# Performance work log

Measured on AMD Instinct MI355X. Metric: run time of the kernel, lower is better.

Reference implementation:

```python
import jax, jax.numpy as jnp
import numpy as np

WS = 8            # window_size
N = WS * WS       # tokens per window = 64
DIM = 512
H = 16            # num_heads
HD = DIM // H     # head_dim = 32
P = 16            # linformer proj_dim
B = 2048          # number of windows (batch * windows per image)


def _relative_position_index(ws: int) -> np.ndarray:
    coords = np.stack(np.meshgrid(np.arange(ws), np.arange(ws), indexing='ij'))  # [2,ws,ws]
    cf = coords.reshape(2, -1)                                                   # [2, N]
    rel = cf[:, :, None] - cf[:, None, :]                                        # [2, N, N]
    rel = rel.transpose(1, 2, 0).astype(np.int64)                                # [N, N, 2]
    rel[:, :, 0] += ws - 1
    rel[:, :, 1] += ws - 1
    rel[:, :, 0] *= 2 * ws - 1
    return rel.sum(-1)  # [N, N]

REL_INDEX = jnp.asarray(_relative_position_index(WS))  # int, [N, N]


def setup_inputs() -> dict:
    key = jax.random.key(0)
    ks = jax.random.split(key, 9)
    s = 0.02
    return {
        'x': jax.random.normal(ks[0], (B, N, DIM), dtype=jnp.float32),
        'w_qkv': jax.random.normal(ks[1], (DIM, 3 * DIM), dtype=jnp.float32) * s,
        'b_qkv': jax.random.normal(ks[2], (3 * DIM,), dtype=jnp.float32) * s,
        'w_proj': jax.random.normal(ks[3], (DIM, DIM), dtype=jnp.float32) * s,
        'b_proj': jax.random.normal(ks[4], (DIM,), dtype=jnp.float32) * s,
        'w_k': jax.random.normal(ks[5], (P, N), dtype=jnp.float32) * s,   # Linear(N -> P), torch weight layout [out,in]
        'w_v': jax.random.normal(ks[6], (P, N), dtype=jnp.float32) * s,
        'bias_table': jax.random.normal(ks[7], ((2 * WS - 1) ** 2, H), dtype=jnp.float32) * s,
    }


def reference(x, w_qkv, b_qkv, w_proj, b_proj, w_k, w_v, bias_table):
    B_, n, c = x.shape
    scale = HD ** -0.5
    qkv = (x @ w_qkv + b_qkv).reshape(B_, n, 3, H, HD)
    qkv = jnp.transpose(qkv, (2, 0, 3, 1, 4))          # [3, B, H, N, hd]
    q, k, v = qkv[0] * scale, qkv[1], qkv[2]           # each [B, H, N, hd]
    # Linformer projection along token axis N -> P
    k = jnp.einsum('bhnd,pn->bhpd', k, w_k)            # [B, H, P, hd]
    v = jnp.einsum('bhnd,pn->bhpd', v, w_v)            # [B, H, P, hd]
    attn = jnp.einsum('bhnd,bhpd->bhnp', q, k)         # [B, H, N, P]
    # relative position bias gather, sliced to projected length P
    bias = bias_table[REL_INDEX.reshape(-1)].reshape(n, n, H)  # [N, N, H]
    bias = jnp.transpose(bias, (2, 0, 1))[None, :, :, :attn.shape[-1]]  # [1, H, N, P]
    attn = jax.nn.softmax(attn + bias, axis=-1)
    out = jnp.einsum('bhnp,bhpd->bhnd', attn, v)       # [B, H, N, hd]
    out = jnp.transpose(out, (0, 2, 1, 3)).reshape(B_, n, c)
    return out @ w_proj + b_proj
```

## Files before the change

### kernel.cpp

```cpp
#include <hip/hip_runtime.h>

typedef __bf16 bf16;
typedef __attribute__((ext_vector_type(8))) __bf16 bf16x8;
typedef __attribute__((ext_vector_type(4))) __bf16 bf16x4;
typedef __attribute__((ext_vector_type(4))) float f32x4;
typedef __attribute__((ext_vector_type(4))) short s16x4;

#define SCALE 0.17677669529663687f

__device__ __forceinline__ f32x4 mfma16(bf16x8 a, bf16x8 b, f32x4 c) {
  return __builtin_amdgcn_mfma_f32_16x16x32_bf16(a, b, c, 0, 0, 0);
}

__device__ __forceinline__ f32x4 mfma16k16(bf16x4 a, bf16x4 b, f32x4 c) {
#if __has_builtin(__builtin_amdgcn_mfma_f32_16x16x16bf16_1k)
  return __builtin_amdgcn_mfma_f32_16x16x16bf16_1k(
      __builtin_bit_cast(s16x4, a), __builtin_bit_cast(s16x4, b), c, 0, 0, 0);
#else
  asm("v_mfma_f32_16x16x16_bf16 %0, %1, %2, %0" : "+v"(c) : "v"(a), "v"(b));
  return c;
#endif
}

__global__ void prep_weights(const float* __restrict__ w_qkv,
                             const float* __restrict__ w_proj,
                             bf16* __restrict__ wt, bf16* __restrict__ wpt) {
  __shared__ float tile[32][33];
  int b = blockIdx.x;
  const float* src; bf16* dst; int C, tk, tc;
  if (b < 768) {
    src = w_qkv; dst = wt; C = 1536; tk = (b & 15) * 32; tc = (b >> 4) * 32;
  } else {
    b -= 768; src = w_proj; dst = wpt; C = 512; tk = (b & 15) * 32; tc = (b >> 4) * 32;
  }
  int tx = threadIdx.x & 31, ty = threadIdx.x >> 5;
#pragma unroll
  for (int i = 0; i < 4; i++)
    tile[ty + i * 8][tx] = src[(size_t)(tk + ty + i * 8) * C + tc + tx];
  __syncthreads();
#pragma unroll
  for (int i = 0; i < 4; i++)
    dst[(size_t)(tc + ty + i * 8) * 512 + tk + tx] = (bf16)tile[tx][ty + i * 8];
}

__launch_bounds__(512, 2)
__global__ void ewattn(const float* __restrict__ x,
                       const float* __restrict__ b_qkv,
                       const float* __restrict__ w_k,
                       const float* __restrict__ w_v,
                       const float* __restrict__ bias_table,
                       const float* __restrict__ b_proj,
                       const bf16* __restrict__ wt,
                       const bf16* __restrict__ wpt,
                       float* __restrict__ out) {
  __shared__ bf16 xs[64][520];
  __shared__ bf16 xk[16][520];
  __shared__ bf16 xv[16][520];
  __shared__ bf16 wkl[16][72];
  __shared__ bf16 wvl[16][72];
  __shared__ float rs[32];
  __shared__ bf16 qs[8][64][40];
  __shared__ bf16 kps[8][16][40];

  const int tid  = threadIdx.x;
  const int lane = tid & 63;
  const int wid  = tid >> 6;
  const int l15  = lane & 15;
  const int quad = lane >> 4;
  const int win  = blockIdx.x;
  const float* xw = x + (size_t)win * (64 * 512);

  for (int i = tid; i < 64 * 64; i += 512) {
    int r = i >> 6, c8 = (i & 63) * 8;
    float4 v0 = *reinterpret_cast<const float4*>(xw + r * 512 + c8);
    float4 v1 = *reinterpret_cast<const float4*>(xw + r * 512 + c8 + 4);
    bf16x8 p;
    p[0] = (bf16)v0.x; p[1] = (bf16)v0.y; p[2] = (bf16)v0.z; p[3] = (bf16)v0.w;
    p[4] = (bf16)v1.x; p[5] = (bf16)v1.y; p[6] = (bf16)v1.z; p[7] = (bf16)v1.w;
    *reinterpret_cast<bf16x8*>(&xs[r][c8]) = p;
  }
  for (int i = tid; i < 1024; i += 512) {
    int p = i >> 6, n = i & 63;
    wkl[p][n] = (bf16)w_k[i];
    wvl[p][n] = (bf16)w_v[i];
  }
  if (tid < 16) {
    float sk = 0.f, sv = 0.f;
#pragma unroll
    for (int n = 0; n < 64; n++) { sk += w_k[tid * 64 + n]; sv += w_v[tid * 64 + n]; }
    rs[tid] = sk; rs[16 + tid] = sv;
  }
  __syncthreads();

  {
    f32x4 ak[4], av[4];
#pragma unroll
    for (int i = 0; i < 4; i++) { ak[i] = f32x4{0.f,0.f,0.f,0.f}; av[i] = f32x4{0.f,0.f,0.f,0.f}; }
#pragma unroll
    for (int kt = 0; kt < 2; kt++) {
      bf16x8 aK = *(const bf16x8*)&wkl[l15][kt * 32 + quad * 8];
      bf16x8 aV = *(const bf16x8*)&wvl[l15][kt * 32 + quad * 8];
      int n0 = kt * 32 + quad * 8;
#pragma unroll
      for (int nt = 0; nt < 4; nt++) {
        int c = wid * 64 + nt * 16 + l15;
        bf16x8 bb;
#pragma unroll
        for (int j = 0; j < 8; j++) bb[j] = xs[n0 + j][c];
        ak[nt] = mfma16(aK, bb, ak[nt]);
        av[nt] = mfma16(aV, bb, av[nt]);
      }
    }
#pragma unroll
    for (int nt = 0; nt < 4; nt++) {
      int c = wid * 64 + nt * 16 + l15;
#pragma unroll
      for (int r = 0; r < 4; r++) {
        xk[quad * 4 + r][c] = (bf16)ak[nt][r];
        xv[quad * 4 + r][c] = (bf16)av[nt][r];
      }
    }
  }

  bf16x4 qb[4][4];
  {
    f32x4 qacc[4][4];
#pragma unroll
    for (int nt = 0; nt < 4; nt++)
#pragma unroll
      for (int mt = 0; mt < 4; mt++) qacc[nt][mt] = f32x4{0.f,0.f,0.f,0.f};
    for (int kt = 0; kt < 16; kt++) {
      bf16x8 af[4];
#pragma unroll
      for (int mt = 0; mt < 4; mt++)
        af[mt] = *(const bf16x8*)&xs[mt * 16 + l15][kt * 32 + quad * 8];
#pragma unroll
      for (int nt = 0; nt < 4; nt++) {
        int c = wid * 64 + nt * 16 + l15;
        bf16x8 bb = *(const bf16x8*)&wt[(size_t)c * 512 + kt * 32 + quad * 8];
#pragma unroll
        for (int mt = 0; mt < 4; mt++)
          qacc[nt][mt] = mfma16(af[mt], bb, qacc[nt][mt]);
      }
    }
#pragma unroll
    for (int nt = 0; nt < 4; nt++) {
      float bq = b_qkv[wid * 64 + nt * 16 + l15];
#pragma unroll
      for (int mt = 0; mt < 4; mt++)
#pragma unroll
        for (int r = 0; r < 4; r++)
          qb[nt][mt][r] = (bf16)((qacc[nt][mt][r] + bq) * SCALE);
    }
  }
  __syncthreads();

  float rsk[4], rsv[4];
#pragma unroll
  for (int j = 0; j < 4; j++) { rsk[j] = rs[quad * 4 + j]; rsv[j] = rs[16 + quad * 4 + j]; }

  for (int hi = 0; hi < 2; hi++) {
    const int h = wid * 2 + hi;

    f32x4 kp[2], vp[2];
    kp[0] = kp[1] = vp[0] = vp[1] = f32x4{0.f,0.f,0.f,0.f};
    for (int kt = 0; kt < 16; kt++) {
      bf16x8 aK = *(const bf16x8*)&xk[l15][kt * 32 + quad * 8];
      bf16x8 aV = *(const bf16x8*)&xv[l15][kt * 32 + quad * 8];
#pragma unroll
      for (int nt = 0; nt < 2; nt++) {
        int ck = 512 + h * 32 + nt * 16 + l15;
        int cv = 1024 + h * 32 + nt * 16 + l15;
        bf16x8 bk = *(const bf16x8*)&wt[(size_t)ck * 512 + kt * 32 + quad * 8];
        bf16x8 bv = *(const bf16x8*)&wt[(size_t)cv * 512 + kt * 32 + quad * 8];
        kp[nt] = mfma16(aK, bk, kp[nt]);
        vp[nt] = mfma16(aV, bv, vp[nt]);
      }
    }
#pragma unroll
    for (int nt = 0; nt < 2; nt++) {
      float bk = b_qkv[512 + h * 32 + nt * 16 + l15];
#pragma unroll
      for (int r = 0; r < 4; r++)
        kps[wid][quad * 4 + r][nt * 16 + l15] = (bf16)(kp[nt][r] + rsk[r] * bk);
    }
    bf16x4 bvf[2];
#pragma unroll
    for (int nd = 0; nd < 2; nd++) {
      float bv = b_qkv[1024 + h * 32 + nd * 16 + l15];
#pragma unroll
      for (int j = 0; j < 4; j++)
        bvf[nd][j] = (bf16)(vp[nd][j] + rsv[j] * bv);
    }

#pragma unroll
    for (int nn = 0; nn < 2; nn++)
#pragma unroll
      for (int mt = 0; mt < 4; mt++)
#pragma unroll
        for (int r = 0; r < 4; r++)
          qs[wid][mt * 16 + quad * 4 + r][nn * 16 + l15] = qb[hi * 2 + nn][mt][r];

    f32x4 at[4];
    {
      bf16x8 bk2 = *(const bf16x8*)&kps[wid][l15][quad * 8];
#pragma unroll
      for (int mt = 0; mt < 4; mt++) {
        bf16x8 aq = *(const bf16x8*)&qs[wid][mt * 16 + l15][quad * 8];
        at[mt] = mfma16(aq, bk2, f32x4{0.f,0.f,0.f,0.f});
      }
    }

    float pr[4][4];
#pragma unroll
    for (int mt = 0; mt < 4; mt++) {
#pragma unroll
      for (int r = 0; r < 4; r++) {
        int n = mt * 16 + quad * 4 + r;
        int rel = ((n >> 3) - (l15 >> 3) + 7) * 15 + ((n & 7) - (l15 & 7) + 7);
        float e = __expf(at[mt][r] + bias_table[rel * 16 + h]);
        float s = e;
        s += __shfl_xor(s, 1); s += __shfl_xor(s, 2);
        s += __shfl_xor(s, 4); s += __shfl_xor(s, 8);
        pr[mt][r] = e * __builtin_amdgcn_rcpf(s);
      }
    }

#pragma unroll
    for (int mt = 0; mt < 4; mt++)
#pragma unroll
      for (int r = 0; r < 4; r++)
        qs[wid][mt * 16 + quad * 4 + r][l15] = (bf16)pr[mt][r];

    f32x4 ov[2][4];
#pragma unroll
    for (int mt = 0; mt < 4; mt++) {
      bf16x4 ap = *(const bf16x4*)&qs[wid][mt * 16 + l15][quad * 4];
#pragma unroll
      for (int nd = 0; nd < 2; nd++)
        ov[nd][mt] = mfma16k16(ap, bvf[nd], f32x4{0.f,0.f,0.f,0.f});
    }
#pragma unroll
    for (int nd = 0; nd < 2; nd++)
#pragma unroll
      for (int mt = 0; mt < 4; mt++)
#pragma unroll
        for (int r = 0; r < 4; r++)
          xs[mt * 16 + quad * 4 + r][h * 32 + nd * 16 + l15] = (bf16)ov[nd][mt][r];
  }
  __syncthreads();

  {
    f32x4 oacc[4][4];
#pragma unroll
    for (int nt = 0; nt < 4; nt++)
#pragma unroll
      for (int mt = 0; mt < 4; mt++) oacc[nt][mt] = f32x4{0.f,0.f,0.f,0.f};
    for (int kt = 0; kt < 16; kt++) {
      bf16x8 af[4];
#pragma unroll
      for (int mt = 0; mt < 4; mt++)
        af[mt] = *(const bf16x8*)&xs[mt * 16 + l15][kt * 32 + quad * 8];
#pragma unroll
      for (int nt = 0; nt < 4; nt++) {
        int c = wid * 64 + nt * 16 + l15;
        bf16x8 bb = *(const bf16x8*)&wpt[(size_t)c * 512 + kt * 32 + quad * 8];
#pragma unroll
        for (int mt = 0; mt < 4; mt++)
          oacc[nt][mt] = mfma16(af[mt], bb, oacc[nt][mt]);
      }
    }
    float* ow = out + (size_t)win * (64 * 512);
#pragma unroll
    for (int nt = 0; nt < 4; nt++) {
      int c = wid * 64 + nt * 16 + l15;
      float bp = b_proj[c];
#pragma unroll
      for (int mt = 0; mt < 4; mt++)
#pragma unroll
        for (int r = 0; r < 4; r++)
          ow[(size_t)(mt * 16 + quad * 4 + r) * 512 + c] = oacc[nt][mt][r] + bp;
    }
  }
}

extern "C" void kernel_launch(void* const* d_in, const int* in_sizes, int n_in,
                              void* d_out, int out_size, void* d_ws, size_t ws_size,
                              hipStream_t stream) {
  const float* x          = (const float*)d_in[0];
  const float* w_qkv      = (const float*)d_in[1];
  const float* b_qkv      = (const float*)d_in[2];
  const float* w_proj     = (const float*)d_in[3];
  const float* b_proj     = (const float*)d_in[4];
  const float* w_k        = (const float*)d_in[5];
  const float* w_v        = (const float*)d_in[6];
  const float* bias_table = (const float*)d_in[7];
  (void)in_sizes; (void)n_in; (void)out_size; (void)ws_size;

  bf16* wt  = (bf16*)d_ws;
  bf16* wpt = wt + 1536 * 512;

  prep_weights<<<1024, 256, 0, stream>>>(w_qkv, w_proj, wt, wpt);
  ewattn<<<2048, 512, 0, stream>>>(x, b_qkv, w_k, w_v, bias_table, b_proj,
                                   wt, wpt, (float*)d_out);
}
```

Baseline: 1.082 ms.

## Use 16 waves per window with one head per wave and register-resident attention

Doubles the block to 1024 threads so each wave owns one head and a 32-column slice of the QKV and output projections. It computes Q transposed (weights as the A operand), so the attention scores and the P·V product can be fed straight from MFMA accumulators in registers. This removes the per-wave qs/kps shared-memory staging and its round trips. The larger block halves per-wave register and tile work, but LDS use per block (~80KB for xs/xk/xv) may cap residency. The launch-bounds request of 4 blocks per CU may also force register spilling.

```diff
diff --git a/kernel.cpp b/kernel.cpp
--- a/kernel.cpp
+++ b/kernel.cpp
@@ -43,7 +43,7 @@
     dst[(size_t)(tc + ty + i * 8) * 512 + tk + tx] = (bf16)tile[tx][ty + i * 8];
 }
 
-__launch_bounds__(512, 2)
+__launch_bounds__(1024, 4)
 __global__ void ewattn(const float* __restrict__ x,
                        const float* __restrict__ b_qkv,
                        const float* __restrict__ w_k,
@@ -59,8 +59,6 @@
   __shared__ bf16 wkl[16][72];
   __shared__ bf16 wvl[16][72];
   __shared__ float rs[32];
-  __shared__ bf16 qs[8][64][40];
-  __shared__ bf16 kps[8][16][40];
 
   const int tid  = threadIdx.x;
   const int lane = tid & 63;
@@ -70,7 +68,7 @@
   const int win  = blockIdx.x;
   const float* xw = x + (size_t)win * (64 * 512);
 
-  for (int i = tid; i < 64 * 64; i += 512) {
+  for (int i = tid; i < 64 * 64; i += 1024) {
     int r = i >> 6, c8 = (i & 63) * 8;
     float4 v0 = *reinterpret_cast<const float4*>(xw + r * 512 + c8);
     float4 v1 = *reinterpret_cast<const float4*>(xw + r * 512 + c8 + 4);
@@ -79,10 +77,10 @@
     p[4] = (bf16)v1.x; p[5] = (bf16)v1.y; p[6] = (bf16)v1.z; p[7] = (bf16)v1.w;
     *reinterpret_cast<bf16x8*>(&xs[r][c8]) = p;
   }
-  for (int i = tid; i < 1024; i += 512) {
-    int p = i >> 6, n = i & 63;
-    wkl[p][n] = (bf16)w_k[i];
-    wvl[p][n] = (bf16)w_v[i];
+  {
+    int p = tid >> 6, n = tid & 63;
+    wkl[p][n] = (bf16)w_k[tid];
+    wvl[p][n] = (bf16)w_v[tid];
   }
   if (tid < 16) {
     float sk = 0.f, sv = 0.f;
@@ -93,17 +91,17 @@
   __syncthreads();
 
   {
-    f32x4 ak[4], av[4];
-#pragma unroll
-    for (int i = 0; i < 4; i++) { ak[i] = f32x4{0.f,0.f,0.f,0.f}; av[i] = f32x4{0.f,0.f,0.f,0.f}; }
+    f32x4 ak[2], av[2];
+#pragma unroll
+    for (int i = 0; i < 2; i++) { ak[i] = f32x4{0.f,0.f,0.f,0.f}; av[i] = f32x4{0.f,0.f,0.f,0.f}; }
 #pragma unroll
     for (int kt = 0; kt < 2; kt++) {
       bf16x8 aK = *(const bf16x8*)&wkl[l15][kt * 32 + quad * 8];
       bf16x8 aV = *(const bf16x8*)&wvl[l15][kt * 32 + quad * 8];
       int n0 = kt * 32 + quad * 8;
 #pragma unroll
-      for (int nt = 0; nt < 4; nt++) {
-        int c = wid * 64 + nt * 16 + l15;
+      for (int nt = 0; nt < 2; nt++) {
+        int c = wid * 32 + nt * 16 + l15;
         bf16x8 bb;
 #pragma unroll
         for (int j = 0; j < 8; j++) bb[j] = xs[n0 + j][c];
@@ -112,8 +110,8 @@
       }
     }
 #pragma unroll
-    for (int nt = 0; nt < 4; nt++) {
-      int c = wid * 64 + nt * 16 + l15;
+    for (int nt = 0; nt < 2; nt++) {
+      int c = wid * 32 + nt * 16 + l15;
 #pragma unroll
       for (int r = 0; r < 4; r++) {
         xk[quad * 4 + r][c] = (bf16)ak[nt][r];
@@ -122,164 +120,127 @@
     }
   }
 
-  bf16x4 qb[4][4];
-  {
-    f32x4 qacc[4][4];
-#pragma unroll
-    for (int nt = 0; nt < 4; nt++)
-#pragma unroll
-      for (int mt = 0; mt < 4; mt++) qacc[nt][mt] = f32x4{0.f,0.f,0.f,0.f};
+  bf16x4 qb[2][4];
+  {
+    f32x4 qacc[2][4];
+#pragma unroll
+    for (int ct = 0; ct < 2; ct++)
+#pragma unroll
+      for (int tt = 0; tt < 4; tt++) qacc[ct][tt] = f32x4{0.f,0.f,0.f,0.f};
+    for (int kt = 0; kt < 16; kt++) {
+      bf16x8 aw[2];
+#pragma unroll
+      for (int ct = 0; ct < 2; ct++)
+        aw[ct] = *(const bf16x8*)&wt[(size_t)(wid * 32 + ct * 16 + l15) * 512 + kt * 32 + quad * 8];
+      bf16x8 bx[4];
+#pragma unroll
+      for (int tt = 0; tt < 4; tt++)
+        bx[tt] = *(const bf16x8*)&xs[tt * 16 + l15][kt * 32 + quad * 8];
+#pragma unroll
+      for (int ct = 0; ct < 2; ct++)
+#pragma unroll
+        for (int tt = 0; tt < 4; tt++)
+          qacc[ct][tt] = mfma16(aw[ct], bx[tt], qacc[ct][tt]);
+    }
+#pragma unroll
+    for (int ct = 0; ct < 2; ct++)
+#pragma unroll
+      for (int tt = 0; tt < 4; tt++)
+#pragma unroll
+        for (int r = 0; r < 4; r++)
+          qb[ct][tt][r] = (bf16)((qacc[ct][tt][r] +
+                                  b_qkv[wid * 32 + ct * 16 + quad * 4 + r]) * SCALE);
+  }
+  __syncthreads();
+
+  const int h = wid;
+  f32x4 kpa[2], vpa[2];
+  kpa[0] = kpa[1] = vpa[0] = vpa[1] = f32x4{0.f,0.f,0.f,0.f};
+  for (int kt = 0; kt < 16; kt++) {
+    bf16x8 xkf = *(const bf16x8*)&xk[l15][kt * 32 + quad * 8];
+    bf16x8 xvf = *(const bf16x8*)&xv[l15][kt * 32 + quad * 8];
+#pragma unroll
+    for (int nt = 0; nt < 2; nt++) {
+      bf16x8 wkf = *(const bf16x8*)&wt[(size_t)(512  + h * 32 + nt * 16 + l15) * 512 + kt * 32 + quad * 8];
+      bf16x8 wvf = *(const bf16x8*)&wt[(size_t)(1024 + h * 32 + nt * 16 + l15) * 512 + kt * 32 + quad * 8];
+      kpa[nt] = mfma16(wkf, xkf, kpa[nt]);
+      vpa[nt] = mfma16(xvf, wvf, vpa[nt]);
+    }
+  }
+  float rskl = rs[l15];
+  float rsvr[4];
+#pragma unroll
+  for (int r = 0; r < 4; r++) rsvr[r] = rs[16 + quad * 4 + r];
+  bf16x4 kpf[2], bvf[2];
+#pragma unroll
+  for (int nt = 0; nt < 2; nt++) {
+    float bvb = b_qkv[1024 + h * 32 + nt * 16 + l15];
+#pragma unroll
+    for (int r = 0; r < 4; r++) {
+      kpf[nt][r] = (bf16)(kpa[nt][r] + rskl * b_qkv[512 + h * 32 + nt * 16 + quad * 4 + r]);
+      bvf[nt][r] = (bf16)(vpa[nt][r] + rsvr[r] * bvb);
+    }
+  }
+
+#pragma unroll
+  for (int tt = 0; tt < 4; tt++) {
+    f32x4 att = mfma16k16(kpf[0], qb[0][tt], f32x4{0.f,0.f,0.f,0.f});
+    att = mfma16k16(kpf[1], qb[1][tt], att);
+    int n = tt * 16 + l15;
+    float e[4], s = 0.f;
+#pragma unroll
+    for (int r = 0; r < 4; r++) {
+      int p = quad * 4 + r;
+      int rel = ((n >> 3) - (p >> 3) + 7) * 15 + ((n & 7) - (p & 7) + 7);
+      e[r] = __expf(att[r] + bias_table[rel * 16 + h]);
+      s += e[r];
+    }
+    s += __shfl_xor(s, 16); s += __shfl_xor(s, 32);
+    float rc = __builtin_amdgcn_rcpf(s);
+    bf16x4 ap;
+#pragma unroll
+    for (int r = 0; r < 4; r++) ap[r] = (bf16)(e[r] * rc);
+#pragma unroll
+    for (int nd = 0; nd < 2; nd++) {
+      f32x4 ov = mfma16k16(ap, bvf[nd], f32x4{0.f,0.f,0.f,0.f});
+#pragma unroll
+      for (int r = 0; r < 4; r++)
+        xs[tt * 16 + quad * 4 + r][h * 32 + nd * 16 + l15] = (bf16)ov[r];
+    }
+  }
+  __syncthreads();
+
+  {
+    f32x4 oacc[4][2];
+#pragma unroll
+    for (int mt = 0; mt < 4; mt++)
+#pragma unroll
+      for (int nt = 0; nt < 2; nt++) oacc[mt][nt] = f32x4{0.f,0.f,0.f,0.f};
     for (int kt = 0; kt < 16; kt++) {
       bf16x8 af[4];
 #pragma unroll
       for (int mt = 0; mt < 4; mt++)
         af[mt] = *(const bf16x8*)&xs[mt * 16 + l15][kt * 32 + quad * 8];
-#pragma unroll
-      for (int nt = 0; nt < 4; nt++) {
-        int c = wid * 64 + nt * 16 + l15;
-        bf16x8 bb = *(const bf16x8*)&wt[(size_t)c * 512 + kt * 32 + quad * 8];
-#pragma unroll
-        for (int mt = 0; mt < 4; mt++)
-          qacc[nt][mt] = mfma16(af[mt], bb, qacc[nt][mt]);
-      }
-    }
-#pragma unroll
-    for (int nt = 0; nt < 4; nt++) {
-      float bq = b_qkv[wid * 64 + nt * 16 + l15];
+      bf16x8 bw[2];
+#pragma unroll
+      for (int nt = 0; nt < 2; nt++)
+        bw[nt] = *(const bf16x8*)&wpt[(size_t)(wid * 32 + nt * 16 + l15) * 512 + kt * 32 + quad * 8];
 #pragma unroll
       for (int mt = 0; mt < 4; mt++)
 #pragma unroll
+        for (int nt = 0; nt < 2; nt++)
+          oacc[mt][nt] = mfma16(af[mt], bw[nt], oacc[mt][nt]);
+    }
+    float* ow = out + (size_t)win * (64 * 512);
+#pragma unroll
+    for (int nt = 0; nt < 2; nt++) {
+      int c = wid * 32 + nt * 16 + l15;
+      float bp = b_proj[c];
+#pragma unroll
+      for (int mt = 0; mt < 4; mt++)
+#pragma unroll
         for (int r = 0; r < 4; r++)
-          qb[nt][mt][r] = (bf16)((qacc[nt][mt][r] + bq) * SCALE);
-    }
-  }
-  __syncthreads();
-
-  float rsk[4], rsv[4];
-#pragma unroll
-  for (int j = 0; j < 4; j++) { rsk[j] = rs[quad * 4 + j]; rsv[j] = rs[16 + quad * 4 + j]; }
-
-  for (int hi = 0; hi < 2; hi++) {
-    const int h = wid * 2 + hi;
-
-    f32x4 kp[2], vp[2];
-    kp[0] = kp[1] = vp[0] = vp[1] = f32x4{0.f,0.f,0.f,0.f};
-    for (int kt = 0; kt < 16; kt++) {
-      bf16x8 aK = *(const bf16x8*)&xk[l15][kt * 32 + quad * 8];
-      bf16x8 aV = *(const bf16x8*)&xv[l15][kt * 32 + quad * 8];
-#pragma unroll
-      for (int nt = 0; nt < 2; nt++) {
-        int ck = 512 + h * 32 + nt * 16 + l15;
-        int cv = 1024 + h * 32 + nt * 16 + l15;
-        bf16x8 bk = *(const bf16x8*)&wt[(size_t)ck * 512 + kt * 32 + quad * 8];
-        bf16x8 bv = *(const bf16x8*)&wt[(size_t)cv * 512 + kt * 32 + quad * 8];
-        kp[nt] = mfma16(aK, bk, kp[nt]);
-        vp[nt] = mfma16(aV, bv, vp[nt]);
-      }
-    }
-#pragma unroll
-    for (int nt = 0; nt < 2; nt++) {
-      float bk = b_qkv[512 + h * 32 + nt * 16 + l15];
-#pragma unroll
-      for (int r = 0; r < 4; r++)
-        kps[wid][quad * 4 + r][nt * 16 + l15] = (bf16)(kp[nt][r] + rsk[r] * bk);
-    }
-    bf16x4 bvf[2];
-#pragma unroll
-    for (int nd = 0; nd < 2; nd++) {
-      float bv = b_qkv[1024 + h * 32 + nd * 16 + l15];
-#pragma unroll
-      for (int j = 0; j < 4; j++)
-        bvf[nd][j] = (bf16)(vp[nd][j] + rsv[j] * bv);
-    }
-
-#pragma unroll
-    for (int nn = 0; nn < 2; nn++)
-#pragma unroll
-      for (int mt = 0; mt < 4; mt++)
-#pragma unroll
-        for (int r = 0; r < 4; r++)
-          qs[wid][mt * 16 + quad * 4 + r][nn * 16 + l15] = qb[hi * 2 + nn][mt][r];
-
-    f32x4 at[4];
-    {
-      bf16x8 bk2 = *(const bf16x8*)&kps[wid][l15][quad * 8];
-#pragma unroll
-      for (int mt = 0; mt < 4; mt++) {
-        bf16x8 aq = *(const bf16x8*)&qs[wid][mt * 16 + l15][quad * 8];
-        at[mt] = mfma16(aq, bk2, f32x4{0.f,0.f,0.f,0.f});
-      }
-    }
-
-    float pr[4][4];
-#pragma unroll
-    for (int mt = 0; mt < 4; mt++) {
-#pragma unroll
-      for (int r = 0; r < 4; r++) {
-        int n = mt * 16 + quad * 4 + r;
-        int rel = ((n >> 3) - (l15 >> 3) + 7) * 15 + ((n & 7) - (l15 & 7) + 7);
-        float e = __expf(at[mt][r] + bias_table[rel * 16 + h]);
-        float s = e;
-        s += __shfl_xor(s, 1); s += __shfl_xor(s, 2);
-        s += __shfl_xor(s, 4); s += __shfl_xor(s, 8);
-        pr[mt][r] = e * __builtin_amdgcn_rcpf(s);
-      }
-    }
-
-#pragma unroll
-    for (int mt = 0; mt < 4; mt++)
-#pragma unroll
-      for (int r = 0; r < 4; r++)
-        qs[wid][mt * 16 + quad * 4 + r][l15] = (bf16)pr[mt][r];
-
-    f32x4 ov[2][4];
-#pragma unroll
-    for (int mt = 0; mt < 4; mt++) {
-      bf16x4 ap = *(const bf16x4*)&qs[wid][mt * 16 + l15][quad * 4];
-#pragma unroll
-      for (int nd = 0; nd < 2; nd++)
-        ov[nd][mt] = mfma16k16(ap, bvf[nd], f32x4{0.f,0.f,0.f,0.f});
-    }
-#pragma unroll
-    for (int nd = 0; nd < 2; nd++)
-#pragma unroll
-      for (int mt = 0; mt < 4; mt++)
-#pragma unroll
-        for (int r = 0; r < 4; r++)
-          xs[mt * 16 + quad * 4 + r][h * 32 + nd * 16 + l15] = (bf16)ov[nd][mt][r];
-  }
-  __syncthreads();
-
-  {
-    f32x4 oacc[4][4];
-#pragma unroll
-    for (int nt = 0; nt < 4; nt++)
-#pragma unroll
-      for (int mt = 0; mt < 4; mt++) oacc[nt][mt] = f32x4{0.f,0.f,0.f,0.f};
-    for (int kt = 0; kt < 16; kt++) {
-      bf16x8 af[4];
-#pragma unroll
-      for (int mt = 0; mt < 4; mt++)
-        af[mt] = *(const bf16x8*)&xs[mt * 16 + l15][kt * 32 + quad * 8];
-#pragma unroll
-      for (int nt = 0; nt < 4; nt++) {
-        int c = wid * 64 + nt * 16 + l15;
-        bf16x8 bb = *(const bf16x8*)&wpt[(size_t)c * 512 + kt * 32 + quad * 8];
-#pragma unroll
-        for (int mt = 0; mt < 4; mt++)
-          oacc[nt][mt] = mfma16(af[mt], bb, oacc[nt][mt]);
-      }
-    }
-    float* ow = out + (size_t)win * (64 * 512);
-#pragma unroll
-    for (int nt = 0; nt < 4; nt++) {
-      int c = wid * 64 + nt * 16 + l15;
-      float bp = b_proj[c];
-#pragma unroll
-      for (int mt = 0; mt < 4; mt++)
-#pragma unroll
-        for (int r = 0; r < 4; r++)
-          ow[(size_t)(mt * 16 + quad * 4 + r) * 512 + c] = oacc[nt][mt][r] + bp;
+          ow[(size_t)(mt * 16 + quad * 4 + r) * 512 + c] = oacc[mt][nt][r] + bp;
     }
   }
 }
@@ -301,6 +262,6 @@
   bf16* wpt = wt + 1536 * 512;
 
   prep_weights<<<1024, 256, 0, stream>>>(w_qkv, w_proj, wt, wpt);
-  ewattn<<<2048, 512, 0, stream>>>(x, b_qkv, w_k, w_v, bias_table, b_proj,
-                                   wt, wpt, (float*)d_out);
-}
+  ewattn<<<2048, 1024, 0, stream>>>(x, b_qkv, w_k, w_v, bias_table, b_proj,
+                                    wt, wpt, (float*)d_out);
+}
```

Measured after the change: 933.5 us. -13.7%, faster.
